# Optimization experiments

Hardware: AMD Instinct MI355X
Metric: run time of the kernel (lower is better)

The kernel has to match this reference:

```python
import jax, jax.numpy as jnp
import numpy as np

NUM_HEADS = 16  # init kwarg num_attention_heads


def setup_inputs() -> dict:
    key = jax.random.key(0)
    k1, k2, k3, k4 = jax.random.split(key, 4)
    B, T, E = 2, 2048, 1024
    query = jax.random.normal(k1, (B, T, E), dtype=jnp.float32)
    key_t = jax.random.normal(k2, (B, T, E), dtype=jnp.float32)
    value = jax.random.normal(k3, (B, T, E), dtype=jnp.float32)
    # final output projection (nn.Linear(hidden, hidden, bias=False)); torch stores [out,in]
    W_out = jax.random.normal(k4, (E, E), dtype=jnp.float32) * 0.02
    return {"query": query, "key": key_t, "value": value, "W_out": W_out}


def reference(query, key, value, W_out):
    # NOTE: in the source, the per-head q_i/k_i/v_i linear projections are
    # overwritten by reshapes of the raw inputs, so the qs/ks/vs weights are
    # dead code. Every head computes identical output; mean over heads is a
    # no-op. We reproduce that exact math here.
    B, T, E = query.shape
    H = NUM_HEADS
    d = E // H  # head_dim; also d_k used in the 1/sqrt(d_k) scaling

    def split_heads(x):  # [B,T,E] -> [B,H,T,d]
        return x.reshape(B, T, H, d).transpose(0, 2, 1, 3)

    q = split_heads(query)
    k = split_heads(key)
    v = split_heads(value)

    scale = jnp.sqrt(jnp.asarray(d, dtype=jnp.float32))
    scores = jnp.einsum('bhtd,bhsd->bhts', q, k) / scale  # [B,H,T,T]
    attn = jax.nn.softmax(scores, axis=-1)
    head = jnp.einsum('bhts,bhsd->bhtd', attn, v)         # [B,H,T,d]
    head = head.transpose(0, 2, 1, 3).reshape(B, T, E)    # concat heads

    # mean over H identical head outputs == head; final linear (no bias)
    outputs = head @ W_out.T                              # [B,T,E]
    # mean over H identical attention maps == attn, returned as [B*H,T,T]
    attention = attn.reshape(B * H, T, T)
    return outputs, attention
```

## Files before the change

kernel.cpp:

```cpp
#include <hip/hip_runtime.h>
#include <hip/hip_fp16.h>

#define B_NUM  2
#define T_DIM  2048
#define E_DIM  1024
#define H_NUM  16
#define D_HEAD 64
#define BH_NUM (B_NUM * H_NUM)
#define NT     (T_DIM / 64)

using half8  = __attribute__((ext_vector_type(8))) _Float16;
using half4v = __attribute__((ext_vector_type(4))) _Float16;
using f32x4  = __attribute__((ext_vector_type(4))) float;

#define AS1 __attribute__((address_space(1)))
#define AS3 __attribute__((address_space(3)))

#define QSCALE 0.18033688011112042f

#define BAR_VM(N)                                                       \
    do {                                                                \
        asm volatile("s_waitcnt vmcnt(" #N ")" ::: "memory");           \
        __builtin_amdgcn_s_barrier();                                   \
        __builtin_amdgcn_sched_barrier(0);                              \
    } while (0)

__device__ __forceinline__ void bar_plain() {
    __builtin_amdgcn_s_barrier();
    __builtin_amdgcn_sched_barrier(0);
}

__global__ void cast_f16_kernel(const float* __restrict__ in,
                                _Float16* __restrict__ out, int n4) {
    int stride = gridDim.x * blockDim.x;
    for (int i = blockIdx.x * blockDim.x + threadIdx.x; i < n4; i += stride) {
        float4 v = reinterpret_cast<const float4*>(in)[i];
        half4v h;
        h[0] = (_Float16)v.x; h[1] = (_Float16)v.y;
        h[2] = (_Float16)v.z; h[3] = (_Float16)v.w;
        reinterpret_cast<half4v*>(out)[i] = h;
    }
}

__global__ void transpose_v_kernel(const float* __restrict__ V,
                                   _Float16* __restrict__ Vt) {
    __shared__ float tile[64][65];
    int s0 = blockIdx.x * 64;
    int bh = blockIdx.y;
    int b = bh >> 4, h = bh & 15;
    int t = threadIdx.x;

    int row = t >> 2;
    int c0  = (t & 3) * 16;
    const float* src = V + ((size_t)(b * T_DIM + s0 + row)) * E_DIM + h * D_HEAD + c0;
#pragma unroll
    for (int j = 0; j < 16; j += 4) {
        float4 v = *reinterpret_cast<const float4*>(src + j);
        tile[row][c0 + j + 0] = v.x;
        tile[row][c0 + j + 1] = v.y;
        tile[row][c0 + j + 2] = v.z;
        tile[row][c0 + j + 3] = v.w;
    }
    __syncthreads();

    int d  = t >> 2;
    int sc = (t & 3) * 16;
    half8 h0, h1;
#pragma unroll
    for (int j = 0; j < 8; ++j) {
        h0[j] = (_Float16)tile[sc + j][d];
        h1[j] = (_Float16)tile[sc + 8 + j][d];
    }
    _Float16* dst = Vt + ((size_t)(bh * D_HEAD + d)) * T_DIM + s0 + sc;
    *reinterpret_cast<half8*>(dst)     = h0;
    *reinterpret_cast<half8*>(dst + 8) = h1;
}

__device__ __forceinline__ void stage_gl(const _Float16* __restrict__ g,
                                         size_t stride, _Float16* lds,
                                         int w, int lane) {
    int r0 = lane >> 3;
    int c  = (lane & 7) ^ r0;
#pragma unroll
    for (int j = 0; j < 2; ++j) {
        int r = (w + 4 * j) * 8 + r0;
        const _Float16* src = g + (size_t)r * stride + c * 8;
        _Float16* dst = lds + (w + 4 * j) * 512;
        __builtin_amdgcn_global_load_lds((const AS1 void*)src, (AS3 void*)dst,
                                         16, 0, 0);
    }
}

__device__ __forceinline__ half8 read_frag64(const _Float16* lds, int row, int chunk) {
    int csw = chunk ^ (row & 7);
    return *reinterpret_cast<const half8*>(lds + row * 64 + csw * 8);
}

__global__ __launch_bounds__(256) void attn_kernel(
        const float* __restrict__ Q, const _Float16* __restrict__ Kh,
        const _Float16* __restrict__ Vt, float* __restrict__ attn_out,
        _Float16* __restrict__ head_h) {
    __shared__ __align__(16) _Float16 kbuf[2][64 * 64];
    __shared__ __align__(16) _Float16 vbuf[2][64 * 64];
    __shared__ __align__(16) _Float16 pbuf[4][16 * 64];

    int tid  = threadIdx.x;
    int wq   = tid >> 6;
    int lane = tid & 63;
    int l15  = lane & 15;
    int lg   = lane >> 4;

    int flat = blockIdx.x;
    int bh   = (flat & 7) * 4 + (flat >> 8);
    int qt   = (flat >> 3) & 31;
    int q0   = qt * 64;
    int b = bh >> 4, h = bh & 15;

    const float* qsrc = Q + ((size_t)(b * T_DIM + q0 + wq * 16 + l15)) * E_DIM + h * D_HEAD;
    half8 qfrag[2];
#pragma unroll
    for (int ks = 0; ks < 2; ++ks) {
        float4 a0 = *reinterpret_cast<const float4*>(qsrc + (lg + 4 * ks) * 8);
        float4 a1 = *reinterpret_cast<const float4*>(qsrc + (lg + 4 * ks) * 8 + 4);
        qfrag[ks][0] = (_Float16)(a0.x * QSCALE); qfrag[ks][1] = (_Float16)(a0.y * QSCALE);
        qfrag[ks][2] = (_Float16)(a0.z * QSCALE); qfrag[ks][3] = (_Float16)(a0.w * QSCALE);
        qfrag[ks][4] = (_Float16)(a1.x * QSCALE); qfrag[ks][5] = (_Float16)(a1.y * QSCALE);
        qfrag[ks][6] = (_Float16)(a1.z * QSCALE); qfrag[ks][7] = (_Float16)(a1.w * QSCALE);
    }

    const _Float16* kg = Kh + ((size_t)b * T_DIM) * E_DIM + h * D_HEAD;
    const _Float16* vg = Vt + (size_t)bh * D_HEAD * T_DIM;

#define P1TILE(KB)                                                             \
    {                                                                          \
        f32x4 acc[4];                                                          \
        _Pragma("unroll")                                                      \
        for (int ct = 0; ct < 4; ++ct) acc[ct] = (f32x4){0.f, 0.f, 0.f, 0.f};  \
        _Pragma("unroll")                                                      \
        for (int ks = 0; ks < 2; ++ks)                                         \
            _Pragma("unroll")                                                  \
            for (int ct = 0; ct < 4; ++ct) {                                   \
                half8 kf = read_frag64((KB), ct * 16 + l15, lg + 4 * ks);      \
                acc[ct] = __builtin_amdgcn_mfma_f32_16x16x32_f16(              \
                    kf, qfrag[ks], acc[ct], 0, 0, 0);                          \
            }                                                                  \
        _Pragma("unroll")                                                      \
        for (int ct = 0; ct < 4; ++ct)                                         \
            _Pragma("unroll")                                                  \
            for (int r = 0; r < 4; ++r)                                        \
                lsum += __builtin_amdgcn_exp2f(acc[ct][r]);                    \
    }

    float lsum = 0.0f;
    int cur = 0;
    stage_gl(kg, E_DIM, kbuf[0], wq, lane);
    for (int t = 0; t < NT - 1; ++t) {
        stage_gl(kg + (size_t)(t + 1) * 64 * E_DIM, E_DIM, kbuf[cur ^ 1], wq, lane);
        BAR_VM(2);
        P1TILE(kbuf[cur]);
        bar_plain();
        cur ^= 1;
    }
    BAR_VM(0);
    P1TILE(kbuf[cur]);

    lsum += __shfl_xor(lsum, 16);
    lsum += __shfl_xor(lsum, 32);
    float rl = 1.0f / lsum;

    f32x4 oacc[4];
#pragma unroll
    for (int cd = 0; cd < 4; ++cd) oacc[cd] = (f32x4){0.f, 0.f, 0.f, 0.f};

    float* ab = attn_out + (size_t)bh * T_DIM * T_DIM;
    _Float16* pw = pbuf[wq];
    int myq = q0 + wq * 16 + l15;

    bar_plain();

    cur = 0;
    stage_gl(kg, E_DIM, kbuf[0], wq, lane);
    stage_gl(vg, T_DIM, vbuf[0], wq, lane);
    for (int t = 0; t < NT; ++t) {
        if (t < NT - 1) {
            stage_gl(kg + (size_t)(t + 1) * 64 * E_DIM, E_DIM, kbuf[cur ^ 1], wq, lane);
            stage_gl(vg + (t + 1) * 64, T_DIM, vbuf[cur ^ 1], wq, lane);
        }
        if (t == 0)           BAR_VM(4);
        else if (t < NT - 1)  BAR_VM(8);
        else                  BAR_VM(4);
        const _Float16* kb = kbuf[cur];
        const _Float16* vb = vbuf[cur];

        f32x4 acc[4];
#pragma unroll
        for (int ct = 0; ct < 4; ++ct) acc[ct] = (f32x4){0.f, 0.f, 0.f, 0.f};
#pragma unroll
        for (int ks = 0; ks < 2; ++ks)
#pragma unroll
            for (int ct = 0; ct < 4; ++ct) {
                half8 kf = read_frag64(kb, ct * 16 + l15, lg + 4 * ks);
                acc[ct] = __builtin_amdgcn_mfma_f32_16x16x32_f16(kf, qfrag[ks], acc[ct], 0, 0, 0);
            }

        float* abrow = ab + (size_t)myq * T_DIM + t * 64 + lg * 4;
#pragma unroll
        for (int ct = 0; ct < 4; ++ct) {
            f32x4 p;
            p[0] = __builtin_amdgcn_exp2f(acc[ct][0]) * rl;
            p[1] = __builtin_amdgcn_exp2f(acc[ct][1]) * rl;
            p[2] = __builtin_amdgcn_exp2f(acc[ct][2]) * rl;
            p[3] = __builtin_amdgcn_exp2f(acc[ct][3]) * rl;
            *reinterpret_cast<f32x4*>(abrow + ct * 16) = p;
            half4v ph;
            ph[0] = (_Float16)p[0]; ph[1] = (_Float16)p[1];
            ph[2] = (_Float16)p[2]; ph[3] = (_Float16)p[3];
            int cc = (ct * 4 + lg) ^ l15;
            *reinterpret_cast<half4v*>(pw + l15 * 64 + cc * 4) = ph;
        }

#pragma unroll
        for (int ks = 0; ks < 2; ++ks) {
            int c0 = 2 * (lg + 4 * ks);
            half4v lo = *reinterpret_cast<const half4v*>(pw + l15 * 64 + ((c0)     ^ l15) * 4);
            half4v hi = *reinterpret_cast<const half4v*>(pw + l15 * 64 + ((c0 + 1) ^ l15) * 4);
            half8 pa;
            pa[0] = lo[0]; pa[1] = lo[1]; pa[2] = lo[2]; pa[3] = lo[3];
            pa[4] = hi[0]; pa[5] = hi[1]; pa[6] = hi[2]; pa[7] = hi[3];
#pragma unroll
            for (int cd = 0; cd < 4; ++cd) {
                half8 vf = read_frag64(vb, cd * 16 + l15, lg + 4 * ks);
                oacc[cd] = __builtin_amdgcn_mfma_f32_16x16x32_f16(pa, vf, oacc[cd], 0, 0, 0);
            }
        }
        bar_plain();
        cur ^= 1;
    }

    _Float16* hw = head_h + ((size_t)(b * T_DIM + q0 + wq * 16)) * E_DIM + h * D_HEAD;
#pragma unroll
    for (int cd = 0; cd < 4; ++cd)
#pragma unroll
        for (int r = 0; r < 4; ++r) {
            int qm = lg * 4 + r;
            hw[(size_t)qm * E_DIM + cd * 16 + l15] = (_Float16)oacc[cd][r];
        }
#undef P1TILE
}

__global__ __launch_bounds__(256) void proj_kernel(
        const _Float16* __restrict__ A, const _Float16* __restrict__ Wh,
        float* __restrict__ out) {
    __shared__ __align__(16) _Float16 abuf[2][64 * 64];
    __shared__ __align__(16) _Float16 bbuf[2][64 * 64];

    int tid  = threadIdx.x;
    int wq   = tid >> 6;
    int lane = tid & 63;
    int l15  = lane & 15;
    int lg   = lane >> 4;

    int m0 = blockIdx.x * 64;
    int n0 = blockIdx.y * 64;

    f32x4 acc[4];
#pragma unroll
    for (int ct = 0; ct < 4; ++ct) acc[ct] = (f32x4){0.f, 0.f, 0.f, 0.f};

    int cur = 0;
    stage_gl(A  + (size_t)m0 * E_DIM, E_DIM, abuf[0], wq, lane);
    stage_gl(Wh + (size_t)n0 * E_DIM, E_DIM, bbuf[0], wq, lane);
    for (int t = 0; t < E_DIM / 64; ++t) {
        if (t + 1 < E_DIM / 64) {
            stage_gl(A  + (size_t)m0 * E_DIM + (t + 1) * 64, E_DIM, abuf[cur ^ 1], wq, lane);
            stage_gl(Wh + (size_t)n0 * E_DIM + (t + 1) * 64, E_DIM, bbuf[cur ^ 1], wq, lane);
            BAR_VM(4);
        } else {
            BAR_VM(0);
        }
#pragma unroll
        for (int ks = 0; ks < 2; ++ks) {
            half8 hf = read_frag64(abuf[cur], wq * 16 + l15, lg + 4 * ks);
#pragma unroll
            for (int ct = 0; ct < 4; ++ct) {
                half8 wf = read_frag64(bbuf[cur], ct * 16 + l15, lg + 4 * ks);
                acc[ct] = __builtin_amdgcn_mfma_f32_16x16x32_f16(wf, hf, acc[ct], 0, 0, 0);
            }
        }
        bar_plain();
        cur ^= 1;
    }

    float* orow = out + (size_t)(m0 + wq * 16 + l15) * E_DIM + n0 + lg * 4;
#pragma unroll
    for (int ct = 0; ct < 4; ++ct) {
        f32x4 o;
        o[0] = acc[ct][0]; o[1] = acc[ct][1]; o[2] = acc[ct][2]; o[3] = acc[ct][3];
        *reinterpret_cast<f32x4*>(orow + ct * 16) = o;
    }
}

extern "C" void kernel_launch(void* const* d_in, const int* in_sizes, int n_in,
                              void* d_out, int out_size, void* d_ws, size_t ws_size,
                              hipStream_t stream) {
    const float* q = (const float*)d_in[0];
    const float* k = (const float*)d_in[1];
    const float* v = (const float*)d_in[2];
    const float* w = (const float*)d_in[3];

    float* outs = (float*)d_out;
    float* attn = outs + (size_t)B_NUM * T_DIM * E_DIM;

    char* ws = (char*)d_ws;
    _Float16* Kh = (_Float16*)(ws);
    _Float16* Vt = (_Float16*)(ws + (size_t)(8  << 20));
    _Float16* Wh = (_Float16*)(ws + (size_t)(16 << 20));
    _Float16* Hh = (_Float16*)(ws + (size_t)(18 << 20));

    int nqkv4 = B_NUM * T_DIM * E_DIM / 4;
    int nw4   = E_DIM * E_DIM / 4;

    cast_f16_kernel<<<1024, 256, 0, stream>>>(k, Kh, nqkv4);
    cast_f16_kernel<<<512, 256, 0, stream>>>(w, Wh, nw4);
    transpose_v_kernel<<<dim3(T_DIM / 64, BH_NUM), 256, 0, stream>>>(v, Vt);
    attn_kernel<<<NT * BH_NUM, 256, 0, stream>>>(q, Kh, Vt, attn, Hh);
    proj_kernel<<<dim3((B_NUM * T_DIM) / 64, E_DIM / 64), 256, 0, stream>>>(Hh, Wh, outs);
}
```

Before: 223.6 us.

## Merge cast kernels, deepen pass-1 K prefetch, add MFMA priority hints

```diff
diff --git a/kernel.cpp b/kernel.cpp
--- a/kernel.cpp
+++ b/kernel.cpp
@@ -30,15 +30,21 @@
     __builtin_amdgcn_sched_barrier(0);
 }
 
-__global__ void cast_f16_kernel(const float* __restrict__ in,
-                                _Float16* __restrict__ out, int n4) {
+__global__ void cast_all_kernel(const float* __restrict__ kin,
+                                const float* __restrict__ win,
+                                _Float16* __restrict__ Kh,
+                                _Float16* __restrict__ Wh,
+                                int nk4, int ntot4) {
     int stride = gridDim.x * blockDim.x;
-    for (int i = blockIdx.x * blockDim.x + threadIdx.x; i < n4; i += stride) {
-        float4 v = reinterpret_cast<const float4*>(in)[i];
+    for (int i = blockIdx.x * blockDim.x + threadIdx.x; i < ntot4; i += stride) {
+        const float* src = (i < nk4) ? kin : win;
+        _Float16* dst    = (i < nk4) ? Kh  : Wh;
+        int j            = (i < nk4) ? i   : i - nk4;
+        float4 v = reinterpret_cast<const float4*>(src)[j];
         half4v h;
         h[0] = (_Float16)v.x; h[1] = (_Float16)v.y;
         h[2] = (_Float16)v.z; h[3] = (_Float16)v.w;
-        reinterpret_cast<half4v*>(out)[i] = h;
+        reinterpret_cast<half4v*>(dst)[j] = h;
     }
 }
 
@@ -96,6 +102,18 @@
     return *reinterpret_cast<const half8*>(lds + row * 64 + csw * 8);
 }
 
+__device__ __forceinline__ void load_qfrag(const float* qsrc, int lg, half8* qf) {
+#pragma unroll
+    for (int ks = 0; ks < 2; ++ks) {
+        float4 a0 = *reinterpret_cast<const float4*>(qsrc + (lg + 4 * ks) * 8);
+        float4 a1 = *reinterpret_cast<const float4*>(qsrc + (lg + 4 * ks) * 8 + 4);
+        qf[ks][0] = (_Float16)(a0.x * QSCALE); qf[ks][1] = (_Float16)(a0.y * QSCALE);
+        qf[ks][2] = (_Float16)(a0.z * QSCALE); qf[ks][3] = (_Float16)(a0.w * QSCALE);
+        qf[ks][4] = (_Float16)(a1.x * QSCALE); qf[ks][5] = (_Float16)(a1.y * QSCALE);
+        qf[ks][6] = (_Float16)(a1.z * QSCALE); qf[ks][7] = (_Float16)(a1.w * QSCALE);
+    }
+}
+
 __global__ __launch_bounds__(256) void attn_kernel(
         const float* __restrict__ Q, const _Float16* __restrict__ Kh,
         const _Float16* __restrict__ Vt, float* __restrict__ attn_out,
@@ -118,15 +136,7 @@
 
     const float* qsrc = Q + ((size_t)(b * T_DIM + q0 + wq * 16 + l15)) * E_DIM + h * D_HEAD;
     half8 qfrag[2];
-#pragma unroll
-    for (int ks = 0; ks < 2; ++ks) {
-        float4 a0 = *reinterpret_cast<const float4*>(qsrc + (lg + 4 * ks) * 8);
-        float4 a1 = *reinterpret_cast<const float4*>(qsrc + (lg + 4 * ks) * 8 + 4);
-        qfrag[ks][0] = (_Float16)(a0.x * QSCALE); qfrag[ks][1] = (_Float16)(a0.y * QSCALE);
-        qfrag[ks][2] = (_Float16)(a0.z * QSCALE); qfrag[ks][3] = (_Float16)(a0.w * QSCALE);
-        qfrag[ks][4] = (_Float16)(a1.x * QSCALE); qfrag[ks][5] = (_Float16)(a1.y * QSCALE);
-        qfrag[ks][6] = (_Float16)(a1.z * QSCALE); qfrag[ks][7] = (_Float16)(a1.w * QSCALE);
-    }
+    load_qfrag(qsrc, lg, qfrag);
 
     const _Float16* kg = Kh + ((size_t)b * T_DIM) * E_DIM + h * D_HEAD;
     const _Float16* vg = Vt + (size_t)bh * D_HEAD * T_DIM;
@@ -152,17 +162,32 @@
     }
 
     float lsum = 0.0f;
-    int cur = 0;
-    stage_gl(kg, E_DIM, kbuf[0], wq, lane);
-    for (int t = 0; t < NT - 1; ++t) {
-        stage_gl(kg + (size_t)(t + 1) * 64 * E_DIM, E_DIM, kbuf[cur ^ 1], wq, lane);
-        BAR_VM(2);
-        P1TILE(kbuf[cur]);
-        bar_plain();
-        cur ^= 1;
-    }
-    BAR_VM(0);
-    P1TILE(kbuf[cur]);
+    stage_gl(kg,                        E_DIM, kbuf[0], wq, lane);
+    stage_gl(kg + (size_t)64 * E_DIM,   E_DIM, kbuf[1], wq, lane);
+    for (int tt = 0; tt < NT / 2; tt += 2) {
+        {
+            const _Float16* nb = kg + (size_t)(2 * tt + 2) * 64 * E_DIM;
+            stage_gl(nb,                      E_DIM, vbuf[0], wq, lane);
+            stage_gl(nb + (size_t)64 * E_DIM, E_DIM, vbuf[1], wq, lane);
+            BAR_VM(4);
+            P1TILE(kbuf[0]);
+            P1TILE(kbuf[1]);
+            bar_plain();
+        }
+        {
+            if (tt + 2 < NT / 2) {
+                const _Float16* nb = kg + (size_t)(2 * tt + 4) * 64 * E_DIM;
+                stage_gl(nb,                      E_DIM, kbuf[0], wq, lane);
+                stage_gl(nb + (size_t)64 * E_DIM, E_DIM, kbuf[1], wq, lane);
+                BAR_VM(4);
+            } else {
+                BAR_VM(0);
+            }
+            P1TILE(vbuf[0]);
+            P1TILE(vbuf[1]);
+            bar_plain();
+        }
+    }
 
     lsum += __shfl_xor(lsum, 16);
     lsum += __shfl_xor(lsum, 32);
@@ -176,9 +201,7 @@
     _Float16* pw = pbuf[wq];
     int myq = q0 + wq * 16 + l15;
 
-    bar_plain();
-
-    cur = 0;
+    int cur = 0;
     stage_gl(kg, E_DIM, kbuf[0], wq, lane);
     stage_gl(vg, T_DIM, vbuf[0], wq, lane);
     for (int t = 0; t < NT; ++t) {
@@ -195,6 +218,7 @@
         f32x4 acc[4];
 #pragma unroll
         for (int ct = 0; ct < 4; ++ct) acc[ct] = (f32x4){0.f, 0.f, 0.f, 0.f};
+        __builtin_amdgcn_s_setprio(1);
 #pragma unroll
         for (int ks = 0; ks < 2; ++ks)
 #pragma unroll
@@ -202,6 +226,7 @@
                 half8 kf = read_frag64(kb, ct * 16 + l15, lg + 4 * ks);
                 acc[ct] = __builtin_amdgcn_mfma_f32_16x16x32_f16(kf, qfrag[ks], acc[ct], 0, 0, 0);
             }
+        __builtin_amdgcn_s_setprio(0);
 
         float* abrow = ab + (size_t)myq * T_DIM + t * 64 + lg * 4;
 #pragma unroll
@@ -219,6 +244,7 @@
             *reinterpret_cast<half4v*>(pw + l15 * 64 + cc * 4) = ph;
         }
 
+        __builtin_amdgcn_s_setprio(1);
 #pragma unroll
         for (int ks = 0; ks < 2; ++ks) {
             int c0 = 2 * (lg + 4 * ks);
@@ -233,6 +259,7 @@
                 oacc[cd] = __builtin_amdgcn_mfma_f32_16x16x32_f16(pa, vf, oacc[cd], 0, 0, 0);
             }
         }
+        __builtin_amdgcn_s_setprio(0);
         bar_plain();
         cur ^= 1;
     }
@@ -317,11 +344,10 @@
     _Float16* Wh = (_Float16*)(ws + (size_t)(16 << 20));
     _Float16* Hh = (_Float16*)(ws + (size_t)(18 << 20));
 
-    int nqkv4 = B_NUM * T_DIM * E_DIM / 4;
-    int nw4   = E_DIM * E_DIM / 4;
-
-    cast_f16_kernel<<<1024, 256, 0, stream>>>(k, Kh, nqkv4);
-    cast_f16_kernel<<<512, 256, 0, stream>>>(w, Wh, nw4);
+    int nk4 = B_NUM * T_DIM * E_DIM / 4;
+    int nw4 = E_DIM * E_DIM / 4;
+
+    cast_all_kernel<<<1280, 256, 0, stream>>>(k, w, Kh, Wh, nk4, nk4 + nw4);
     transpose_v_kernel<<<dim3(T_DIM / 64, BH_NUM), 256, 0, stream>>>(v, Vt);
     attn_kernel<<<NT * BH_NUM, 256, 0, stream>>>(q, Kh, Vt, attn, Hh);
     proj_kernel<<<dim3((B_NUM * T_DIM) / 64, E_DIM / 64), 256, 0, stream>>>(Hh, Wh, outs);
```

New measurement: 206.3 us. 1.08x faster.
